# Kernel optimization log

Hardware: AMD Instinct MI355X
Metric: run time of the kernel (lower is better)

The kernel has to match this reference:

```python
import jax, jax.numpy as jnp
import numpy as np

B, T, U, V, H = 64, 800, 100, 80, 512
KA, KO = 10, 20
ATT_MULT = 0.05


def setup_inputs() -> dict:
    key = jax.random.key(0)
    ks = jax.random.split(key, 16)
    s = 0.05
    inp = {
        'chars': jax.random.randint(ks[0], (B, U), 0, V, dtype=jnp.int32),
        'chars_mask': jnp.ones((B, U), jnp.float32),
        'strokes': jax.random.normal(ks[1], (B, T, 3), jnp.float32),
        'strokes_mask': jnp.ones((B, T), jnp.float32),
        # lstm_0: LSTMCell(3+V -> H), PyTorch gate order i,f,g,o; biases fused
        'W_ih0': jax.random.normal(ks[2], (4 * H, 3 + V), jnp.float32) * s,
        'W_hh0': jax.random.normal(ks[3], (4 * H, H), jnp.float32) * s,
        'b0': jnp.zeros((4 * H,), jnp.float32),
        # attention linear: H -> 3*KA
        'W_att': jax.random.normal(ks[4], (3 * KA, H), jnp.float32) * s,
        'b_att': jnp.zeros((3 * KA,), jnp.float32),
        # lstm_1: (3+V+H -> H)
        'W_ih1': jax.random.normal(ks[5], (4 * H, 3 + V + H), jnp.float32) * s,
        'W_hh1': jax.random.normal(ks[6], (4 * H, H), jnp.float32) * s,
        'b1': jnp.zeros((4 * H,), jnp.float32),
        # lstm_2: (3+V+H -> H)
        'W_ih2': jax.random.normal(ks[7], (4 * H, 3 + V + H), jnp.float32) * s,
        'W_hh2': jax.random.normal(ks[8], (4 * H, H), jnp.float32) * s,
        'b2': jnp.zeros((4 * H,), jnp.float32),
        # fc: 3H -> 6*KO + 1
        'W_fc': jax.random.normal(ks[9], (6 * KO + 1, 3 * H), jnp.float32) * s,
        'b_fc': jnp.zeros((6 * KO + 1,), jnp.float32),
    }
    return inp


def _lstm_step(h, c, x, W_ih, W_hh, b):
    gates = x @ W_ih.T + h @ W_hh.T + b
    i, f, g, o = jnp.split(gates, 4, axis=-1)
    c = jax.nn.sigmoid(f) * c + jax.nn.sigmoid(i) * jnp.tanh(g)
    h = jax.nn.sigmoid(o) * jnp.tanh(c)
    return h, c


def _lstm_layer(x_btd, W_ih, W_hh, b):
    # x_btd: [B, T, D] -> [B, T, H]
    def step(carry, x_t):
        h, c = carry
        h, c = _lstm_step(h, c, x_t, W_ih, W_hh, b)
        return (h, c), h
    h0 = jnp.zeros((x_btd.shape[0], H), x_btd.dtype)
    c0 = jnp.zeros_like(h0)
    _, hs = jax.lax.scan(step, (h0, c0), jnp.swapaxes(x_btd, 0, 1))
    return jnp.swapaxes(hs, 0, 1)


def _forward(chars, chars_mask, strokes, strokes_mask,
             W_ih0, W_hh0, b0, W_att, b_att,
             W_ih1, W_hh1, b1, W_ih2, W_hh2, b2, W_fc, b_fc):
    ctx = jax.nn.one_hot(chars, V, dtype=jnp.float32) * chars_mask[..., None]  # [B,U,V]
    u = jnp.arange(U, dtype=jnp.float32)  # [U]

    def step(carry, x_t):
        h0, c0, w_t, k_t = carry
        h0, c0 = _lstm_step(h0, c0, jnp.concatenate([x_t, w_t], -1), W_ih0, W_hh0, b0)
        abk = jnp.exp(h0 @ W_att.T + b_att)  # [B, 3*KA]
        alpha, beta, kappa = jnp.split(abk, 3, axis=-1)  # each [B, KA]
        kappa = kappa * ATT_MULT + k_t
        # phi: [B, U]
        phi = jnp.sum(alpha[:, None, :] * jnp.exp(-beta[:, None, :] * (kappa[:, None, :] - u[None, :, None]) ** 2), axis=-1)
        phi = phi * chars_mask
        w_t = jnp.einsum('bu,buv->bv', phi, ctx)
        return (h0, c0, w_t, kappa), (h0, w_t)

    init = (jnp.zeros((B, H)), jnp.zeros((B, H)), jnp.zeros((B, V)), jnp.zeros((B, KA)))
    _, (h0_seq, w_seq) = jax.lax.scan(step, init, jnp.swapaxes(strokes, 0, 1))
    lstm0_out = jnp.swapaxes(h0_seq, 0, 1)      # [B,T,H]
    att_out = jnp.swapaxes(w_seq, 0, 1)         # [B,T,V]

    lstm1_out = _lstm_layer(jnp.concatenate([strokes, att_out, lstm0_out], -1), W_ih1, W_hh1, b1)
    lstm2_out = _lstm_layer(jnp.concatenate([strokes, att_out, lstm1_out], -1), W_ih2, W_hh2, b2)

    last = jnp.concatenate([lstm0_out, lstm1_out, lstm2_out], -1) @ W_fc.T + b_fc  # [B,T,6*KO+1]
    mu, log_sigma, pi, rho, eos = jnp.split(last, [2 * KO, 4 * KO, 5 * KO, 6 * KO], axis=-1)
    rho = jnp.tanh(rho)
    log_pi = jax.nn.log_softmax(pi, axis=-1)
    eos = jax.nn.sigmoid(-eos)
    # packed output: [log_pi | mu | log_sigma | rho | eos] -> [B,T,6*KO+1]
    return jnp.concatenate([log_pi, mu, log_sigma, rho, eos], axis=-1)


def reference(chars, chars_mask, strokes, strokes_mask,
              W_ih0, W_hh0, b0, W_att, b_att,
              W_ih1, W_hh1, b1, W_ih2, W_hh2, b2, W_fc, b_fc):
    return _forward(chars, chars_mask, strokes, strokes_mask,
                    W_ih0, W_hh0, b0, W_att, b_att,
                    W_ih1, W_hh1, b1, W_ih2, W_hh2, b2, W_fc, b_fc)
```

## Files before the change

### kernel.cpp

```cpp
#include <hip/hip_runtime.h>


#define TT   800
#define NOUT 121
#define NEG  (-1073741824)
typedef unsigned long long u64;
typedef unsigned int u32;
typedef __attribute__((ext_vector_type(8))) short short8v;
typedef __attribute__((ext_vector_type(4))) float float4v;

#define RSLOT   65536
#define RWSLOT  12288
#define OFF_SEQ 0
#define OFF_R0  16384
#define OFF_R1  (OFF_R0 + 16 * RSLOT)
#define OFF_R2  (OFF_R1 + 16 * RSLOT)
#define OFF_RW  (OFF_R2 + 16 * RSLOT)
#define OFF_WATT (OFF_RW + 16 * RWSLOT)
#define OFF_OV  (OFF_WATT + 65536)
#define ABLK    36864
#define OFF_WA1 (OFF_OV + 801 * 4096)
#define OFF_WA2 (OFF_WA1 + 256 * ABLK)
#define OFF_WFC (OFF_WA2 + 128 * ABLK)
#define OFF_END (OFF_WFC + 8 * 48 * 1024)

#define MFMA_B16(a, b, c) __builtin_amdgcn_mfma_f32_16x16x32_bf16(a, b, c, 0, 0, 0)

__device__ __forceinline__ float sigmf(float x) { return 1.f / (1.f + __expf(-x)); }
__device__ __forceinline__ float tanhf_(float x) { return 1.f - 2.f / (1.f + __expf(2.f * x)); }
__device__ __forceinline__ unsigned short f2bf(float x) {
    u32 u = __float_as_uint(x);
    return (unsigned short)((u + 0x7FFFu + ((u >> 16) & 1u)) >> 16);
}
__device__ __forceinline__ float bf2f(u32 s) { return __uint_as_float(s << 16); }

__device__ __forceinline__ u64 cl64(const u64* p) {
    return __hip_atomic_load(p, __ATOMIC_RELAXED, __HIP_MEMORY_SCOPE_AGENT);
}
__device__ __forceinline__ u32 cl32(const u32* p) {
    return __hip_atomic_load(p, __ATOMIC_RELAXED, __HIP_MEMORY_SCOPE_AGENT);
}
__device__ __forceinline__ void cs32(u32* p, u32 v) {
    __hip_atomic_store(p, v, __ATOMIC_RELAXED, __HIP_MEMORY_SCOPE_AGENT);
}
__device__ __forceinline__ void cs64(u64* p, u64 v) {
    __hip_atomic_store(p, v, __ATOMIC_RELAXED, __HIP_MEMORY_SCOPE_AGENT);
}

__global__ void prep_zero(u32* ws32) {
    int n = (OFF_WATT - OFF_SEQ) / 4;
    for (int i = blockIdx.x * blockDim.x + threadIdx.x; i < n; i += gridDim.x * blockDim.x) {
        u32 v = 0u;
        if (i < 4096 && (i & 31) == 0) {
            int f = i >> 5;
            if (f >= 104 && f < 128) v = 0x7FFFFFFFu;
        }
        ws32[i] = v;
    }
}
__global__ void prep_ov(const float* __restrict__ strokes, short* __restrict__ dst) {
    int n = 801 * 2048;
    for (int idx = blockIdx.x * blockDim.x + threadIdx.x; idx < n; idx += gridDim.x * blockDim.x) {
        int s = idx >> 11, rem = idx & 2047;
        int t = rem >> 9, lane = (rem >> 3) & 63, j = rem & 7;
        int k = 1088 + (lane >> 4) * 8 + j;
        int b = t * 16 + (lane & 15);
        short v = 0;
        int tt = -1, d = 0;
        if (k >= 1104 && k <= 1106)      { tt = s - 1; d = k - 1104; }
        else if (k >= 1107 && k <= 1109) { tt = s;     d = k - 1107; }
        if (tt >= 0 && tt < TT) v = (short)f2bf(strokes[((size_t)b * TT + tt) * 3 + d]);
        dst[idx] = v;
    }
}
__global__ void prep_watt(const float* __restrict__ W_att, short* __restrict__ dst) {
    int n = 2 * 2 * 16 * 512;
    for (int idx = blockIdx.x * blockDim.x + threadIdx.x; idx < n; idx += gridDim.x * blockDim.x) {
        int part = idx >> 14;
        int mt = (idx >> 13) & 1;
        int c = (idx >> 9) & 15;
        int lane = (idx >> 3) & 63, j = idx & 7;
        int a = mt * 16 + (lane & 15);
        int k = c * 32 + ((lane >> 4) << 3) + j;
        float v = (a < 30) ? W_att[a * 512 + k] : 0.f;
        unsigned short h = f2bf(v);
        if (part) { float r = v - bf2f(h); h = f2bf(r); }
        dst[idx] = (short)h;
    }
}
__global__ void prep_wa1(const float* __restrict__ Wih0, const float* __restrict__ Whh0,
                         const float* __restrict__ Wih1, const float* __restrict__ Whh1,
                         short* __restrict__ dst) {
    int n = 256 * 36 * 512;
    for (int idx = blockIdx.x * blockDim.x + threadIdx.x; idx < n; idx += gridDim.x * blockDim.x) {
        int blk = idx / 18432, rem = idx % 18432;
        int c = rem >> 9, r2 = rem & 511, lane = r2 >> 3, j = r2 & 7;
        int m = lane & 15, q = lane >> 4;
        int k = c * 32 + q * 8 + j;
        int gate = m & 3, hloc = m >> 2;
        float v = 0.f;
        if (blk < 128) {
            int grow = gate * 512 + blk * 4 + hloc;
            if (k >= 512 && k < 1024)       v = Whh0[(size_t)grow * 512 + (k - 512)];
            else if (k >= 1024 && k < 1104) v = Wih0[(size_t)grow * 83 + 3 + (k - 1024)];
            else if (k >= 1107 && k < 1110) v = Wih0[(size_t)grow * 83 + (k - 1107)];
        } else {
            int grow = gate * 512 + (blk - 128) * 4 + hloc;
            if (k < 512)        v = Whh1[(size_t)grow * 512 + k];
            else if (k < 1024)  v = Wih1[(size_t)grow * 595 + 83 + (k - 512)];
            else if (k < 1104)  v = Wih1[(size_t)grow * 595 + 3 + (k - 1024)];
            else if (k < 1107)  v = Wih1[(size_t)grow * 595 + (k - 1104)];
        }
        dst[idx] = (short)f2bf(v);
    }
}
__global__ void prep_wa2(const float* __restrict__ Wih2, const float* __restrict__ Whh2,
                         short* __restrict__ dst) {
    int n = 128 * 36 * 512;
    for (int idx = blockIdx.x * blockDim.x + threadIdx.x; idx < n; idx += gridDim.x * blockDim.x) {
        int blk = idx / 18432, rem = idx % 18432;
        int c = rem >> 9, r2 = rem & 511, lane = r2 >> 3, j = r2 & 7;
        int m = lane & 15, q = lane >> 4;
        int k = c * 32 + q * 8 + j;
        int grow = (m & 3) * 512 + blk * 4 + (m >> 2);
        float v = 0.f;
        if (k < 512)        v = Whh2[(size_t)grow * 512 + k];
        else if (k < 1024)  v = Wih2[(size_t)grow * 595 + 83 + (k - 512)];
        else if (k < 1104)  v = Wih2[(size_t)grow * 595 + 3 + (k - 1024)];
        else if (k < 1107)  v = Wih2[(size_t)grow * 595 + (k - 1104)];
        dst[idx] = (short)f2bf(v);
    }
}
__global__ void prep_wfc(const float* __restrict__ W_fc, short* __restrict__ dst) {
    int n = 8 * 48 * 512;
    for (int idx = blockIdx.x * blockDim.x + threadIdx.x; idx < n; idx += gridDim.x * blockDim.x) {
        int mt = idx / 24576, rem = idx % 24576;
        int c = rem >> 9, r2 = rem & 511, lane = r2 >> 3, j = r2 & 7;
        int o = mt * 16 + (lane & 15);
        int k = c * 32 + (lane >> 4) * 8 + j;
        float v = (o < NOUT) ? W_fc[(size_t)o * 1536 + k] : 0.f;
        dst[idx] = (short)f2bf(v);
    }
}

__device__ __forceinline__ void waitf(u32* SEQ, int i1, int t1, int i2, int t2, int wv) {
    if (wv == 0) {
        int spin = 0;
        while (1) {
            int v1 = (int)cl32(SEQ + i1 * 32);
            int v2 = (int)cl32(SEQ + i2 * 32);
            if (__all((v1 >= t1) & (v2 >= t2))) break;
            if (++spin > (1 << 18)) break;
        }
    }
    __syncthreads();
}
__device__ __forceinline__ void publish(u32* SEQ, int idx, int val) {
    asm volatile("s_waitcnt vmcnt(0)" ::: "memory");
    __syncthreads();
    if (threadIdx.x == 0) cs32(SEQ + idx * 32, (u32)val);
}

__device__ __forceinline__ void store_h(char* slot, int nb, int mt, int nt,
                                        int q, int nn, u32 hb) {
    u32 g1 = (u32)__shfl((int)hb, nn + 16, 64);
    u32 g2 = (u32)__shfl((int)hb, nn + 32, 64);
    u32 g3 = (u32)__shfl((int)hb, nn + 48, 64);
    if (q == 0) {
        int k0 = nb * 16 + mt * 4;
        int ck = k0 >> 5, qq = (k0 >> 3) & 3, j0 = k0 & 7;
        u64 pk = (u64)(hb & 0xFFFFu) | ((u64)(g1 & 0xFFFFu) << 16)
               | ((u64)(g2 & 0xFFFFu) << 32) | ((u64)(g3 & 0xFFFFu) << 48);
        u64* dst = (u64*)(slot + ((((ck * 4 + nt) * 64 + qq * 16 + nn) * 8 + j0) * 2));
        cs64(dst, pk);
    }
}

__device__ __forceinline__ float4v gemm_run(const short* __restrict__ Ab,
                                            const short* __restrict__ pB,
                                            int c0, int cN, float4v acc) {
    short8v a0 = *(const short8v*)(Ab + (size_t)(c0 + 0) * 512);
    short8v a1 = *(const short8v*)(Ab + (size_t)(c0 + 1) * 512);
    short8v a2 = *(const short8v*)(Ab + (size_t)(c0 + 2) * 512);
    short8v a3 = *(const short8v*)(Ab + (size_t)(c0 + 3) * 512);
    short8v a4 = *(const short8v*)(Ab + (size_t)(c0 + 4) * 512);
    short8v a5 = *(const short8v*)(Ab + (size_t)(c0 + 5) * 512);
    short8v a6 = *(const short8v*)(Ab + (size_t)(c0 + 6) * 512);
    short8v a7 = *(const short8v*)(Ab + (size_t)(c0 + 7) * 512);
    int c = c0;
    short8v bv;
#pragma unroll 1
    for (; c + 8 < cN; c += 8) {
        bv = *(const short8v*)(pB + (size_t)(c + 0) * 2048);
        acc = MFMA_B16(a0, bv, acc);
        if (c + 8 < cN)  a0 = *(const short8v*)(Ab + (size_t)(c + 8) * 512);
        bv = *(const short8v*)(pB + (size_t)(c + 1) * 2048);
        acc = MFMA_B16(a1, bv, acc);
        if (c + 9 < cN)  a1 = *(const short8v*)(Ab + (size_t)(c + 9) * 512);
        bv = *(const short8v*)(pB + (size_t)(c + 2) * 2048);
        acc = MFMA_B16(a2, bv, acc);
        if (c + 10 < cN) a2 = *(const short8v*)(Ab + (size_t)(c + 10) * 512);
        bv = *(const short8v*)(pB + (size_t)(c + 3) * 2048);
        acc = MFMA_B16(a3, bv, acc);
        if (c + 11 < cN) a3 = *(const short8v*)(Ab + (size_t)(c + 11) * 512);
        bv = *(const short8v*)(pB + (size_t)(c + 4) * 2048);
        acc = MFMA_B16(a4, bv, acc);
        if (c + 12 < cN) a4 = *(const short8v*)(Ab + (size_t)(c + 12) * 512);
        bv = *(const short8v*)(pB + (size_t)(c + 5) * 2048);
        acc = MFMA_B16(a5, bv, acc);
        if (c + 13 < cN) a5 = *(const short8v*)(Ab + (size_t)(c + 13) * 512);
        bv = *(const short8v*)(pB + (size_t)(c + 6) * 2048);
        acc = MFMA_B16(a6, bv, acc);
        if (c + 14 < cN) a6 = *(const short8v*)(Ab + (size_t)(c + 14) * 512);
        bv = *(const short8v*)(pB + (size_t)(c + 7) * 2048);
        acc = MFMA_B16(a7, bv, acc);
        if (c + 15 < cN) a7 = *(const short8v*)(Ab + (size_t)(c + 15) * 512);
    }
    int r = cN - c;
    bv = *(const short8v*)(pB + (size_t)(c + 0) * 2048);
    acc = MFMA_B16(a0, bv, acc);
    if (r > 1) { bv = *(const short8v*)(pB + (size_t)(c + 1) * 2048); acc = MFMA_B16(a1, bv, acc); }
    if (r > 2) { bv = *(const short8v*)(pB + (size_t)(c + 2) * 2048); acc = MFMA_B16(a2, bv, acc); }
    if (r > 3) { bv = *(const short8v*)(pB + (size_t)(c + 3) * 2048); acc = MFMA_B16(a3, bv, acc); }
    if (r > 4) { bv = *(const short8v*)(pB + (size_t)(c + 4) * 2048); acc = MFMA_B16(a4, bv, acc); }
    if (r > 5) { bv = *(const short8v*)(pB + (size_t)(c + 5) * 2048); acc = MFMA_B16(a5, bv, acc); }
    if (r > 6) { bv = *(const short8v*)(pB + (size_t)(c + 6) * 2048); acc = MFMA_B16(a6, bv, acc); }
    if (r > 7) { bv = *(const short8v*)(pB + (size_t)(c + 7) * 2048); acc = MFMA_B16(a7, bv, acc); }
    return acc;
}

__global__ void __launch_bounds__(1024, 4)
hand_pipeline(const int* __restrict__ chars, const float* __restrict__ chars_mask,
              const float* __restrict__ b_att,
              const float* __restrict__ b0, const float* __restrict__ b1,
              const float* __restrict__ b2, const float* __restrict__ b_fc,
              float* ws, float* __restrict__ out) {
    __shared__ short panel[36 * 4 * 64 * 8];
    char* wsB = (char*)ws;
    u32* SEQ = (u32*)(wsB + OFF_SEQ);
    u64* pan8 = (u64*)panel;
    const int tid = threadIdx.x;
    const int blk = blockIdx.x;
    const int lid = tid & 63;
    const int wv  = __builtin_amdgcn_readfirstlane(tid >> 6);
    const int q   = lid >> 4, nn = lid & 15;
    const int mt  = wv >> 2, nt = wv & 3;
    const int role = blk >> 5;
    const int nb   = blk & 31;

    float* ABK  = (float*)panel;
    float* KAP  = ABK + 2048;
    float* WCTX = KAP + 640;
    unsigned char* CH8 = (unsigned char*)(WCTX + 5184);
    float* M2   = (float*)(CH8 + 6400);
    float* BATT = M2 + 6400;

    for (int i = tid; i < 18432; i += 1024) pan8[i] = 0ull;
    __syncthreads();

    float biasr[4] = {0.f, 0.f, 0.f, 0.f};
    if (role < 3) {
        const float* bp = role == 0 ? b0 : role == 1 ? b1 : b2;
        int hg = nb * 16 + mt * 4 + q;
#pragma unroll
        for (int r = 0; r < 4; ++r) biasr[r] = bp[r * 512 + hg];
    }
    if (role == 0) {
        for (int i = tid; i < 6400; i += 1024) {
            int u2 = i >> 6, b = i & 63;
            CH8[i] = (unsigned char)chars[b * 100 + u2];
            float m = chars_mask[b * 100 + u2];
            M2[i] = m * m;
        }
        if (tid < 640) KAP[tid] = 0.f;
        if (tid < 32) BATT[tid] = (tid < 30) ? b_att[tid] : 0.f;
    }
    __syncthreads();

    const short* WA1 = (const short*)(wsB + OFF_WA1);
    const short* WA2 = (const short*)(wsB + OFF_WA2);
    float cst = 0.f;

    if (role == 0) {
        const short* Ab = WA1 + (size_t)(nb * 4 + mt) * 18432 + lid * 8;
        const short* pB = panel + (size_t)(nt * 64 + lid) * 8;
        for (int s = 0; s <= TT; ++s) {
            if ((s & 7) == 0) waitf(SEQ, 32 + lid, s - 8, 96 + (lid & 7), s - 8, wv);
            {
                const u64* sO = (const u64*)(wsB + OFF_OV + (size_t)s * 4096);
                if (tid < 512) pan8[17408 + tid] = sO[tid];
#pragma unroll
                for (int it = 0; it < 6; ++it) {
                    int i = tid + it * 1024;
                    if (i < 5184) WCTX[i] = 0.f;
                }
            }
            waitf(SEQ, lid & 31, s, lid & 31, NEG, wv);
            {
                const u64* sB = (const u64*)(wsB + OFF_R0 + (size_t)((s - 1) & 15) * RSLOT);
                u64 tb[8];
#pragma unroll
                for (int it = 0; it < 8; ++it) tb[it] = cl64(sB + tid + it * 1024);
#pragma unroll
                for (int it = 0; it < 8; ++it) pan8[8192 + tid + it * 1024] = tb[it];
            }
            __syncthreads();
            const bool actA = (s >= 1);
            float4v acc = {0.f, 0.f, 0.f, 0.f};
            if (wv >= 8) {
                if (s < TT) acc = gemm_run(Ab, pB, 16, 32, acc);
            } else if (actA) {
                const int mta = mt & 1;
                const short* Ah = (const short*)(wsB + OFF_WATT) + (size_t)mta * 8192 + lid * 8;
                const short* Al = Ah + 16384;
                const short* pBA = panel + (size_t)((64 + nt) * 64 + lid) * 8;
                float4v aacc = {0.f, 0.f, 0.f, 0.f};
#pragma unroll 4
                for (int c = 0; c < 16; ++c) {
                    short8v bv = *(const short8v*)(pBA + (size_t)c * 2048);
                    aacc = MFMA_B16(*(const short8v*)(Ah + (size_t)c * 512), bv, aacc);
                    aacc = MFMA_B16(*(const short8v*)(Al + (size_t)c * 512), bv, aacc);
                }
#pragma unroll
                for (int r = 0; r < 4; ++r) {
                    int a = mta * 16 + q * 4 + r;
                    if (a < 30) ABK[a * 64 + nt * 16 + nn] = __expf(aacc[r] + BATT[a]);
                }
            }
            __syncthreads();
            if (actA) {
                const int b = tid & 63;
                float al[10], be[10], kp[10];
#pragma unroll
                for (int ka = 0; ka < 10; ++ka) {
                    al[ka] = ABK[ka * 64 + b];
                    be[ka] = ABK[(10 + ka) * 64 + b];
                    kp[ka] = KAP[ka * 64 + b] + 0.05f * ABK[(20 + ka) * 64 + b];
                }
                for (int i = tid; i < 6400; i += 1024) {
                    float fu = (float)(i >> 6);
                    float ph = 0.f;
#pragma unroll
                    for (int ka = 0; ka < 10; ++ka) {
                        float d = kp[ka] - fu;
                        ph = fmaf(al[ka], __expf(-be[ka] * d * d), ph);
                    }
                    float m2 = M2[i];
                    if (m2 != 0.f) atomicAdd(&WCTX[b * 81 + CH8[i]], ph * m2);
                }
            }
            __syncthreads();
            if (wv < 8) {
                if (s < TT) acc = gemm_run(Ab, pB, 16, 32, acc);
            } else if (actA) {
                const int st = tid - 512;
#pragma unroll
                for (int ii = 0; ii < 2; ++ii) {
                    int i = st + ii * 512;
                    if (i < 640) KAP[i] += 0.05f * ABK[(20 + (i >> 6)) * 64 + (i & 63)];
                }
                for (int idx = st; idx < 6144; idx += 512) {
                    int c = idx >> 11, rem = idx & 2047;
                    int nt2 = rem >> 9, l = (rem >> 3) & 63, j = rem & 7;
                    int k = 1024 + c * 32 + ((l >> 4) << 3) + j;
                    if (k < 1104) {
                        int b = nt2 * 16 + (l & 15);
                        panel[(size_t)(((32 + c) * 4 + nt2) * 64 + l) * 8 + j] =
                            (short)f2bf(WCTX[b * 81 + (k - 1024)]);
                    }
                }
                if (st < 80) {
                    int bsel = st / 40, p = st - bsel * 40;
                    int bb = nb * 2 + bsel;
                    int k = 1024 + p * 2;
                    int lc = (k - 1024) >> 5, qq = (k >> 3) & 3, j = k & 7;
                    char* slot = wsB + OFF_RW + (size_t)((s - 1) & 15) * RWSLOT;
                    u32* dst = (u32*)(slot +
                        ((((lc * 4 + (bb >> 4)) * 64 + qq * 16 + (bb & 15)) * 8 + j) * 2));
                    cs32(dst, (u32)f2bf(WCTX[bb * 81 + 2 * p]) |
                              ((u32)f2bf(WCTX[bb * 81 + 2 * p + 1]) << 16));
                }
            }
            __syncthreads();
            if (s < TT) {
#pragma unroll
                for (int c = 32; c < 35; ++c) {
                    short8v av = *(const short8v*)(Ab + (size_t)c * 512);
                    short8v bv = *(const short8v*)(pB + (size_t)c * 2048);
                    acc = MFMA_B16(av, bv, acc);
                }
                float gi = acc[0] + biasr[0], gf = acc[1] + biasr[1];
                float gg = acc[2] + biasr[2], go = acc[3] + biasr[3];
                cst = sigmf(gf) * cst + sigmf(gi) * tanhf_(gg);
                float h = sigmf(go) * tanhf_(cst);
                store_h(wsB + OFF_R0 + (size_t)(s & 15) * RSLOT, nb, mt, nt, q, nn, f2bf(h));
            }
            publish(SEQ, blk, s + 1);
        }
    } else if (role < 3) {
        const short* Ab = (role == 1 ? WA1 + (size_t)(128 + nb * 4 + mt) * 18432
                                     : WA2 + (size_t)(nb * 4 + mt) * 18432) + lid * 8;
        const short* pB = panel + (size_t)(nt * 64 + lid) * 8;
        for (int t = 0; t < TT; ++t) {
            if ((t & 7) == 0) {
                if (role == 1) waitf(SEQ, 64 + (lid & 31), t - 8, 96 + (lid & 7), t - 8, wv);
                else           waitf(SEQ, 96 + (lid & 7), t - 8, 96 + (lid & 7), NEG, wv);
            }
            if (role == 1) waitf(SEQ, 32 + (lid & 31), t, 32 + (lid & 31), NEG, wv);
            else           waitf(SEQ, 64 + (lid & 31), t, 64 + (lid & 31), NEG, wv);
            const u64* sA = (const u64*)(wsB + (role == 1 ? OFF_R1 : OFF_R2) +
                                         (size_t)((t - 1) & 15) * RSLOT);
            u64 ta[8];
#pragma unroll
            for (int it = 0; it < 8; ++it) ta[it] = cl64(sA + tid + it * 1024);
            if (role == 1) waitf(SEQ, lid & 31, t + 2, lid & 31, NEG, wv);
            else           waitf(SEQ, lid, (lid < 32) ? t + 2 : t + 1, lid & 31, NEG, wv);
            {
                const u64* sB = (role == 1)
                    ? (const u64*)(wsB + OFF_R0 + (size_t)(t & 15) * RSLOT)
                    : (const u64*)(wsB + OFF_R1 + (size_t)(t & 15) * RSLOT);
                const u64* sW = (const u64*)(wsB + OFF_RW + (size_t)(t & 15) * RWSLOT);
                const u64* sO = (const u64*)(wsB + OFF_OV + (size_t)(t + 1) * 4096);
                u64 tb[8];
#pragma unroll
                for (int it = 0; it < 8; ++it) tb[it] = cl64(sB + tid + it * 1024);
                u64 tw = cl64(sW + tid);
                u64 tov = (tid < 512) ? (cl64(sW + 1024 + tid) | sO[tid]) : 0ull;
#pragma unroll
                for (int it = 0; it < 8; ++it) pan8[tid + it * 1024] = ta[it];
#pragma unroll
                for (int it = 0; it < 8; ++it) pan8[8192 + tid + it * 1024] = tb[it];
                pan8[16384 + tid] = tw;
                if (tid < 512) pan8[17408 + tid] = tov;
            }
            __syncthreads();
            {
                float4v acc = {0.f, 0.f, 0.f, 0.f};
                acc = gemm_run(Ab, pB, 0, 35, acc);
                float gi = acc[0] + biasr[0], gf = acc[1] + biasr[1];
                float gg = acc[2] + biasr[2], go = acc[3] + biasr[3];
                cst = sigmf(gf) * cst + sigmf(gi) * tanhf_(gg);
                float h = sigmf(go) * tanhf_(cst);
                store_h(wsB + (role == 1 ? OFF_R1 : OFF_R2) + (size_t)(t & 15) * RSLOT,
                        nb, mt, nt, q, nn, f2bf(h));
            }
            publish(SEQ, blk, t + 1);
        }
    } else {
        const int fcb = blk - 96;
        const int kq = wv >> 2, ntw = wv & 3;
        float* FR = (float*)panel;
        for (int t = 0; t < TT; ++t) {
            waitf(SEQ, lid, t + 1, 64 + (lid & 31), t + 1, wv);
            const char* p0 = wsB + OFF_R0 + (size_t)(t & 15) * RSLOT;
            const char* p1 = wsB + OFF_R1 + (size_t)(t & 15) * RSLOT;
            const char* p2 = wsB + OFF_R2 + (size_t)(t & 15) * RSLOT;
            const int boff = ntw * 1024 + lid * 16;
            auto BLD = [&](int C) -> short8v {
                const char* p = (C < 16) ? p0 + (size_t)C * 4096
                             : (C < 32) ? p1 + (size_t)(C - 16) * 4096
                                        : p2 + (size_t)(C - 32) * 4096;
                const u64* q8 = (const u64*)(p + boff);
                union { u64 w[2]; short8v v; } uu;
                uu.w[0] = cl64(q8); uu.w[1] = cl64(q8 + 1);
                return uu.v;
            };
            const short* Ab = (const short*)(wsB + OFF_WFC) + (size_t)fcb * 24576 + lid * 8;
            const int cb = kq * 12;
            short8v bvv[12];
#pragma unroll
            for (int i = 0; i < 12; ++i) bvv[i] = BLD(cb + i);
            short8v av[6];
#pragma unroll
            for (int i = 0; i < 6; ++i)
                av[i] = *(const short8v*)(Ab + (size_t)(cb + i) * 512);
            float4v acc = {0.f, 0.f, 0.f, 0.f};
#pragma unroll
            for (int i = 0; i < 6; ++i) {
                acc = MFMA_B16(av[i], bvv[i], acc);
                av[i] = *(const short8v*)(Ab + (size_t)(cb + 6 + i) * 512);
            }
#pragma unroll
            for (int i = 0; i < 6; ++i) acc = MFMA_B16(av[i], bvv[6 + i], acc);
#pragma unroll
            for (int r = 0; r < 4; ++r) FR[(wv * 64 + lid) * 4 + r] = acc[r];
            __syncthreads();
            if (kq == 0) {
#pragma unroll
                for (int r = 0; r < 4; ++r)
                    acc[r] = FR[(wv * 64 + lid) * 4 + r] + FR[((wv + 4) * 64 + lid) * 4 + r]
                           + FR[((wv + 8) * 64 + lid) * 4 + r] + FR[((wv + 12) * 64 + lid) * 4 + r];
                const int bb = ntw * 16 + nn;
                float* po = out + ((size_t)bb * TT + t) * NOUT + fcb * 16 + q * 4;
#pragma unroll
                for (int r = 0; r < 4; ++r) {
                    int o = fcb * 16 + q * 4 + r;
                    if (o < NOUT) po[r] = acc[r] + b_fc[o];
                }
            }
            publish(SEQ, blk, t + 1);
        }
    }
}

__global__ void postproc_kernel(float* __restrict__ out) {
    int row  = blockIdx.x * 8 + (threadIdx.x >> 5);
    int lane = threadIdx.x & 31;
    float* r = out + (size_t)row * NOUT;
    float pv = (lane < 20) ? r[80 + lane] : -1e30f;
    float m = pv;
#pragma unroll
    for (int off = 16; off; off >>= 1) m = fmaxf(m, __shfl_xor(m, off, 32));
    float e = (lane < 20) ? __expf(pv - m) : 0.f;
    float sm = e;
#pragma unroll
    for (int off = 16; off; off >>= 1) sm += __shfl_xor(sm, off, 32);
    float logZ = m + __logf(sm);
    float res[4];
    bool wr[4];
    int ps[4];
#pragma unroll
    for (int i = 0; i < 4; ++i) {
        int p = lane + 32 * i;
        ps[i] = p;
        wr[i] = (p < NOUT);
        float x = 0.f;
        if (p < 20)       x = pv - logZ;
        else if (p < 100) { if (wr[i]) x = r[p - 20]; }
        else if (p < 120) x = tanhf_(r[p]);
        else if (p == 120) x = 1.f / (1.f + __expf(r[120]));
        res[i] = x;
    }
#pragma unroll
    for (int i = 0; i < 4; ++i)
        if (wr[i]) r[ps[i]] = res[i];
}

extern "C" void kernel_launch(void* const* d_in, const int* in_sizes, int n_in,
                              void* d_out, int out_size, void* d_ws, size_t ws_size,
                              hipStream_t stream) {
    const int*   chars      = (const int*)d_in[0];
    const float* chars_mask = (const float*)d_in[1];
    const float* strokes    = (const float*)d_in[2];
    const float* W_ih0 = (const float*)d_in[4];
    const float* W_hh0 = (const float*)d_in[5];
    const float* b0    = (const float*)d_in[6];
    const float* W_att = (const float*)d_in[7];
    const float* b_att = (const float*)d_in[8];
    const float* W_ih1 = (const float*)d_in[9];
    const float* W_hh1 = (const float*)d_in[10];
    const float* b1    = (const float*)d_in[11];
    const float* W_ih2 = (const float*)d_in[12];
    const float* W_hh2 = (const float*)d_in[13];
    const float* b2    = (const float*)d_in[14];
    const float* W_fc  = (const float*)d_in[15];
    const float* b_fc  = (const float*)d_in[16];
    float* ws  = (float*)d_ws;
    float* out = (float*)d_out;
    char*  wsB = (char*)d_ws;

    prep_zero<<<512, 256, 0, stream>>>((u32*)ws);
    prep_ov<<<1024, 256, 0, stream>>>(strokes, (short*)(wsB + OFF_OV));
    prep_watt<<<64, 256, 0, stream>>>(W_att, (short*)(wsB + OFF_WATT));
    prep_wa1<<<2048, 256, 0, stream>>>(W_ih0, W_hh0, W_ih1, W_hh1, (short*)(wsB + OFF_WA1));
    prep_wa2<<<1024, 256, 0, stream>>>(W_ih2, W_hh2, (short*)(wsB + OFF_WA2));
    prep_wfc<<<256, 256, 0, stream>>>(W_fc, (short*)(wsB + OFF_WFC));

    hand_pipeline<<<104, 1024, 0, stream>>>(chars, chars_mask, b_att,
                                            b0, b1, b2, b_fc, ws, out);
    postproc_kernel<<<(64 * TT) / 8, 256, 0, stream>>>(out);
}
```

Measured before the change: 16.17 ms.

## Keep per-wave weight fragments resident in registers across all timesteps

Weight A-fragments for the LSTM gate GEMMs, attention projection and FC output are loaded once into VGPR arrays before the time loop instead of being re-read from global memory every step. The generic gemm_run helper is removed and replaced with fully unrolled MFMA loops over the register-held fragments. This removes repeated global/L2 weight traffic on the serial recurrence critical path. It raises register pressure considerably (up to 35 short8v per thread, i.e. 140 VGPRs) under 1024-thread launch bounds, which risks spilling.

```diff
diff --git a/kernel.cpp b/kernel.cpp
--- a/kernel.cpp
+++ b/kernel.cpp
@@ -176,59 +176,6 @@
     }
 }
 
-__device__ __forceinline__ float4v gemm_run(const short* __restrict__ Ab,
-                                            const short* __restrict__ pB,
-                                            int c0, int cN, float4v acc) {
-    short8v a0 = *(const short8v*)(Ab + (size_t)(c0 + 0) * 512);
-    short8v a1 = *(const short8v*)(Ab + (size_t)(c0 + 1) * 512);
-    short8v a2 = *(const short8v*)(Ab + (size_t)(c0 + 2) * 512);
-    short8v a3 = *(const short8v*)(Ab + (size_t)(c0 + 3) * 512);
-    short8v a4 = *(const short8v*)(Ab + (size_t)(c0 + 4) * 512);
-    short8v a5 = *(const short8v*)(Ab + (size_t)(c0 + 5) * 512);
-    short8v a6 = *(const short8v*)(Ab + (size_t)(c0 + 6) * 512);
-    short8v a7 = *(const short8v*)(Ab + (size_t)(c0 + 7) * 512);
-    int c = c0;
-    short8v bv;
-#pragma unroll 1
-    for (; c + 8 < cN; c += 8) {
-        bv = *(const short8v*)(pB + (size_t)(c + 0) * 2048);
-        acc = MFMA_B16(a0, bv, acc);
-        if (c + 8 < cN)  a0 = *(const short8v*)(Ab + (size_t)(c + 8) * 512);
-        bv = *(const short8v*)(pB + (size_t)(c + 1) * 2048);
-        acc = MFMA_B16(a1, bv, acc);
-        if (c + 9 < cN)  a1 = *(const short8v*)(Ab + (size_t)(c + 9) * 512);
-        bv = *(const short8v*)(pB + (size_t)(c + 2) * 2048);
-        acc = MFMA_B16(a2, bv, acc);
-        if (c + 10 < cN) a2 = *(const short8v*)(Ab + (size_t)(c + 10) * 512);
-        bv = *(const short8v*)(pB + (size_t)(c + 3) * 2048);
-        acc = MFMA_B16(a3, bv, acc);
-        if (c + 11 < cN) a3 = *(const short8v*)(Ab + (size_t)(c + 11) * 512);
-        bv = *(const short8v*)(pB + (size_t)(c + 4) * 2048);
-        acc = MFMA_B16(a4, bv, acc);
-        if (c + 12 < cN) a4 = *(const short8v*)(Ab + (size_t)(c + 12) * 512);
-        bv = *(const short8v*)(pB + (size_t)(c + 5) * 2048);
-        acc = MFMA_B16(a5, bv, acc);
-        if (c + 13 < cN) a5 = *(const short8v*)(Ab + (size_t)(c + 13) * 512);
-        bv = *(const short8v*)(pB + (size_t)(c + 6) * 2048);
-        acc = MFMA_B16(a6, bv, acc);
-        if (c + 14 < cN) a6 = *(const short8v*)(Ab + (size_t)(c + 14) * 512);
-        bv = *(const short8v*)(pB + (size_t)(c + 7) * 2048);
-        acc = MFMA_B16(a7, bv, acc);
-        if (c + 15 < cN) a7 = *(const short8v*)(Ab + (size_t)(c + 15) * 512);
-    }
-    int r = cN - c;
-    bv = *(const short8v*)(pB + (size_t)(c + 0) * 2048);
-    acc = MFMA_B16(a0, bv, acc);
-    if (r > 1) { bv = *(const short8v*)(pB + (size_t)(c + 1) * 2048); acc = MFMA_B16(a1, bv, acc); }
-    if (r > 2) { bv = *(const short8v*)(pB + (size_t)(c + 2) * 2048); acc = MFMA_B16(a2, bv, acc); }
-    if (r > 3) { bv = *(const short8v*)(pB + (size_t)(c + 3) * 2048); acc = MFMA_B16(a3, bv, acc); }
-    if (r > 4) { bv = *(const short8v*)(pB + (size_t)(c + 4) * 2048); acc = MFMA_B16(a4, bv, acc); }
-    if (r > 5) { bv = *(const short8v*)(pB + (size_t)(c + 5) * 2048); acc = MFMA_B16(a5, bv, acc); }
-    if (r > 6) { bv = *(const short8v*)(pB + (size_t)(c + 6) * 2048); acc = MFMA_B16(a6, bv, acc); }
-    if (r > 7) { bv = *(const short8v*)(pB + (size_t)(c + 7) * 2048); acc = MFMA_B16(a7, bv, acc); }
-    return acc;
-}
-
 __global__ void __launch_bounds__(1024, 4)
 hand_pipeline(const int* __restrict__ chars, const float* __restrict__ chars_mask,
               const float* __restrict__ b_att,
@@ -284,6 +231,19 @@
     if (role == 0) {
         const short* Ab = WA1 + (size_t)(nb * 4 + mt) * 18432 + lid * 8;
         const short* pB = panel + (size_t)(nt * 64 + lid) * 8;
+        short8v AR[19];
+#pragma unroll
+        for (int c = 0; c < 19; ++c) AR[c] = *(const short8v*)(Ab + (size_t)(16 + c) * 512);
+        short8v AH[16], AL[16];
+        if (wv < 8) {
+            const int mta = mt & 1;
+            const short* Ah = (const short*)(wsB + OFF_WATT) + (size_t)mta * 8192 + lid * 8;
+#pragma unroll
+            for (int c = 0; c < 16; ++c) {
+                AH[c] = *(const short8v*)(Ah + (size_t)c * 512);
+                AL[c] = *(const short8v*)(Ah + 16384 + (size_t)c * 512);
+            }
+        }
         for (int s = 0; s <= TT; ++s) {
             if ((s & 7) == 0) waitf(SEQ, 32 + lid, s - 8, 96 + (lid & 7), s - 8, wv);
             {
@@ -308,18 +268,22 @@
             const bool actA = (s >= 1);
             float4v acc = {0.f, 0.f, 0.f, 0.f};
             if (wv >= 8) {
-                if (s < TT) acc = gemm_run(Ab, pB, 16, 32, acc);
+                if (s < TT) {
+#pragma unroll
+                    for (int c = 0; c < 16; ++c) {
+                        short8v bv = *(const short8v*)(pB + (size_t)(16 + c) * 2048);
+                        acc = MFMA_B16(AR[c], bv, acc);
+                    }
+                }
             } else if (actA) {
                 const int mta = mt & 1;
-                const short* Ah = (const short*)(wsB + OFF_WATT) + (size_t)mta * 8192 + lid * 8;
-                const short* Al = Ah + 16384;
                 const short* pBA = panel + (size_t)((64 + nt) * 64 + lid) * 8;
                 float4v aacc = {0.f, 0.f, 0.f, 0.f};
-#pragma unroll 4
+#pragma unroll
                 for (int c = 0; c < 16; ++c) {
                     short8v bv = *(const short8v*)(pBA + (size_t)c * 2048);
-                    aacc = MFMA_B16(*(const short8v*)(Ah + (size_t)c * 512), bv, aacc);
-                    aacc = MFMA_B16(*(const short8v*)(Al + (size_t)c * 512), bv, aacc);
+                    aacc = MFMA_B16(AH[c], bv, aacc);
+                    aacc = MFMA_B16(AL[c], bv, aacc);
                 }
 #pragma unroll
                 for (int r = 0; r < 4; ++r) {
@@ -351,7 +315,13 @@
             }
             __syncthreads();
             if (wv < 8) {
-                if (s < TT) acc = gemm_run(Ab, pB, 16, 32, acc);
+                if (s < TT) {
+#pragma unroll
+                    for (int c = 0; c < 16; ++c) {
+                        short8v bv = *(const short8v*)(pB + (size_t)(16 + c) * 2048);
+                        acc = MFMA_B16(AR[c], bv, acc);
+                    }
+                }
             } else if (actA) {
                 const int st = tid - 512;
 #pragma unroll
@@ -384,10 +354,9 @@
             __syncthreads();
             if (s < TT) {
 #pragma unroll
-                for (int c = 32; c < 35; ++c) {
-                    short8v av = *(const short8v*)(Ab + (size_t)c * 512);
-                    short8v bv = *(const short8v*)(pB + (size_t)c * 2048);
-                    acc = MFMA_B16(av, bv, acc);
+                for (int c = 16; c < 19; ++c) {
+                    short8v bv = *(const short8v*)(pB + (size_t)(16 + c) * 2048);
+                    acc = MFMA_B16(AR[c], bv, acc);
                 }
                 float gi = acc[0] + biasr[0], gf = acc[1] + biasr[1];
                 float gg = acc[2] + biasr[2], go = acc[3] + biasr[3];
@@ -401,6 +370,9 @@
         const short* Ab = (role == 1 ? WA1 + (size_t)(128 + nb * 4 + mt) * 18432
                                      : WA2 + (size_t)(nb * 4 + mt) * 18432) + lid * 8;
         const short* pB = panel + (size_t)(nt * 64 + lid) * 8;
+        short8v AR[35];
+#pragma unroll
+        for (int c = 0; c < 35; ++c) AR[c] = *(const short8v*)(Ab + (size_t)c * 512);
         for (int t = 0; t < TT; ++t) {
             if ((t & 7) == 0) {
                 if (role == 1) waitf(SEQ, 64 + (lid & 31), t - 8, 96 + (lid & 7), t - 8, wv);
@@ -436,7 +408,11 @@
             __syncthreads();
             {
                 float4v acc = {0.f, 0.f, 0.f, 0.f};
-                acc = gemm_run(Ab, pB, 0, 35, acc);
+#pragma unroll
+                for (int c = 0; c < 35; ++c) {
+                    short8v bv = *(const short8v*)(pB + (size_t)c * 2048);
+                    acc = MFMA_B16(AR[c], bv, acc);
+                }
                 float gi = acc[0] + biasr[0], gf = acc[1] + biasr[1];
                 float gg = acc[2] + biasr[2], go = acc[3] + biasr[3];
                 cst = sigmf(gf) * cst + sigmf(gi) * tanhf_(gg);
@@ -450,6 +426,11 @@
         const int fcb = blk - 96;
         const int kq = wv >> 2, ntw = wv & 3;
         float* FR = (float*)panel;
+        const short* Ab = (const short*)(wsB + OFF_WFC) + (size_t)fcb * 24576 + lid * 8;
+        const int cb = kq * 12;
+        short8v AR[12];
+#pragma unroll
+        for (int i = 0; i < 12; ++i) AR[i] = *(const short8v*)(Ab + (size_t)(cb + i) * 512);
         for (int t = 0; t < TT; ++t) {
             waitf(SEQ, lid, t + 1, 64 + (lid & 31), t + 1, wv);
             const char* p0 = wsB + OFF_R0 + (size_t)(t & 15) * RSLOT;
@@ -465,23 +446,12 @@
                 uu.w[0] = cl64(q8); uu.w[1] = cl64(q8 + 1);
                 return uu.v;
             };
-            const short* Ab = (const short*)(wsB + OFF_WFC) + (size_t)fcb * 24576 + lid * 8;
-            const int cb = kq * 12;
             short8v bvv[12];
 #pragma unroll
             for (int i = 0; i < 12; ++i) bvv[i] = BLD(cb + i);
-            short8v av[6];
-#pragma unroll
-            for (int i = 0; i < 6; ++i)
-                av[i] = *(const short8v*)(Ab + (size_t)(cb + i) * 512);
             float4v acc = {0.f, 0.f, 0.f, 0.f};
 #pragma unroll
-            for (int i = 0; i < 6; ++i) {
-                acc = MFMA_B16(av[i], bvv[i], acc);
-                av[i] = *(const short8v*)(Ab + (size_t)(cb + 6 + i) * 512);
-            }
-#pragma unroll
-            for (int i = 0; i < 6; ++i) acc = MFMA_B16(av[i], bvv[6 + i], acc);
+            for (int i = 0; i < 12; ++i) acc = MFMA_B16(AR[i], bvv[i], acc);
 #pragma unroll
             for (int r = 0; r < 4; ++r) FR[(wv * 64 + lid) * 4 + r] = acc[r];
             __syncthreads();
```

Measured after the change: 24.07 ms. +48.8%, slower.
